# Optimization experiments

Measured on AMD Instinct MI355X. Metric: run time of the kernel, lower is better.

The kernel has to match this reference:

```python
import jax, jax.numpy as jnp
import numpy as np

BS, SEQ, D, H = 2, 2048, 1024, 16
HD = D // H  # head_dim = 64


def setup_inputs() -> dict:
    key = jax.random.key(0)
    kx, kw = jax.random.split(key)
    x = jax.random.normal(kx, (BS, SEQ, D), dtype=jnp.float32)
    # qkv Linear: weight [3D, D] (xavier_normal), bias zeros
    std = float(np.sqrt(2.0 / (D + 3 * D)))
    W_qkv = jax.random.normal(kw, (3 * D, D), dtype=jnp.float32) * std
    b_qkv = jnp.zeros((3 * D,), dtype=jnp.float32)
    return {"x": x, "W_qkv": W_qkv, "b_qkv": b_qkv}


def reference(x, W_qkv, b_qkv):
    bs, seq_len, embed_dim = x.shape
    # fused QKV projection: [bs, seq, 3D]
    qkv = x @ W_qkv.T + b_qkv
    qkv = qkv.reshape(bs, seq_len, 3, H, HD)
    qkv = jnp.transpose(qkv, (2, 0, 3, 1, 4))  # [3, bs, H, seq, HD]
    Q, K, V = qkv[0], qkv[1], qkv[2]
    # past_kv is None -> total_len == seq_len, past_len == 0
    scores = jnp.einsum("bhqd,bhkd->bhqk", Q, K) / jnp.sqrt(jnp.float32(HD))
    # causal mask: True above diagonal -> -inf
    mask = jnp.triu(jnp.ones((seq_len, seq_len), dtype=bool), k=1)
    scores = jnp.where(mask[None, None, :, :], -jnp.inf, scores)
    probs = jax.nn.softmax(scores, axis=-1)
    # attn_dropout = 0.0 (eval) -> identity
    out = jnp.einsum("bhqk,bhkd->bhqd", probs, V)
    out = jnp.transpose(out, (0, 2, 1, 3)).reshape(bs, seq_len, embed_dim)
    return (out, (K, V))
```

## Files before the change

kernel.cpp:

```cpp
#include <hip/hip_runtime.h>

typedef __bf16 bf16_t;
typedef __bf16 bf16x8 __attribute__((ext_vector_type(8)));
typedef float f32x4 __attribute__((ext_vector_type(4)));
typedef unsigned long long u64;

__device__ __forceinline__ unsigned short bfbits(float f) {
  unsigned u = __float_as_uint(f);
  u += 0x7fffu + ((u >> 16) & 1u);
  return (unsigned short)(u >> 16);
}
__device__ __forceinline__ bf16_t f2bf(float f) {
  unsigned short s = bfbits(f);
  union { unsigned short s; bf16_t b; } cv; cv.s = s; return cv.b;
}

__device__ __forceinline__ void gl16(const void* g, void* l) {
  __builtin_amdgcn_global_load_lds(
      (const __attribute__((address_space(1))) void*)g,
      (__attribute__((address_space(3))) void*)l,
      16, 0, 0);
}

__global__ __launch_bounds__(256) void cvt_kernel(const float* __restrict__ x,
                                                  const float* __restrict__ Wf,
                                                  bf16_t* __restrict__ xb,
                                                  bf16_t* __restrict__ wb) {
  const int i = blockIdx.x * 256 + threadIdx.x;
  const float* src; bf16_t* dst; int j;
  if (i < 524288) { j = i; src = x; dst = xb; }
  else            { j = i - 524288; src = Wf; dst = wb; }
  const float4* s = (const float4*)src + (size_t)j * 2;
  float4 a = s[0], b = s[1];
  bf16x8 o;
  o[0] = f2bf(a.x); o[1] = f2bf(a.y); o[2] = f2bf(a.z); o[3] = f2bf(a.w);
  o[4] = f2bf(b.x); o[5] = f2bf(b.y); o[6] = f2bf(b.z); o[7] = f2bf(b.w);
  const int row = j >> 7, jr = j & 127;
  const int dstc = (row << 7) + (jr & ~3) + ((jr & 3) ^ ((row >> 1) & 3));
  *((bf16x8*)dst + dstc) = o;
}

#define GEMM_K 1024
__global__ __launch_bounds__(256) void qkv_gemm(
    const bf16_t* __restrict__ A,
    const bf16_t* __restrict__ B,
    const float* __restrict__ bias,
    float* __restrict__ Ko, float* __restrict__ Vo,
    bf16_t* __restrict__ Qb, bf16_t* __restrict__ Kb,
    bf16_t* __restrict__ Vt,
    int* __restrict__ qcnt)
{
  if (blockIdx.x == 0 && threadIdx.x == 0) *qcnt = 0;
  __shared__ bf16_t lsA[3][4096];
  __shared__ bf16_t lsB[3][4096];
  const int tid = threadIdx.x;
  const int lane = tid & 63;
  const int ln = lane & 15, qd = lane >> 4;
  const int wid = tid >> 6;
  const int wm = wid & 1, wn = wid >> 1;
  const int xcd = blockIdx.x & 7;
  const int j = blockIdx.x >> 3;
  const int bn = xcd * 3 + (j % 3);
  const int bm = j / 3;
  const int m0 = bm * 128, n0 = bn * 128;
  const int qs = qd ^ ((ln >> 1) & 3);

  f32x4 acc[4][4] = {};

  const int c0 = tid, c1 = tid + 256;
  const bf16_t* ga0 = A + (size_t)(m0 + (c0 >> 2)) * GEMM_K + (c0 & 3) * 8;
  const bf16_t* ga1 = A + (size_t)(m0 + (c1 >> 2)) * GEMM_K + (c1 & 3) * 8;
  const bf16_t* gb0 = B + (size_t)(n0 + (c0 >> 2)) * GEMM_K + (c0 & 3) * 8;
  const bf16_t* gb1 = B + (size_t)(n0 + (c1 >> 2)) * GEMM_K + (c1 & 3) * 8;

#define STAGE(t, slot)                                   \
  do {                                                   \
    const int ko_ = (t) * 32;                            \
    gl16(ga0 + ko_, &lsA[(slot)][c0 * 8]);               \
    gl16(ga1 + ko_, &lsA[(slot)][c1 * 8]);               \
    gl16(gb0 + ko_, &lsB[(slot)][c0 * 8]);               \
    gl16(gb1 + ko_, &lsB[(slot)][c1 * 8]);               \
  } while (0)

#define COMPUTE(slot)                                                          \
  do {                                                                         \
    bf16x8 af[4], bf[4];                                                       \
    _Pragma("unroll")                                                          \
    for (int mi = 0; mi < 4; ++mi)                                             \
      af[mi] = *(const bf16x8*)&lsA[(slot)][(wm * 64 + mi * 16 + ln) * 32 + qs * 8]; \
    _Pragma("unroll")                                                          \
    for (int ni = 0; ni < 4; ++ni)                                             \
      bf[ni] = *(const bf16x8*)&lsB[(slot)][(wn * 64 + ni * 16 + ln) * 32 + qs * 8]; \
    _Pragma("unroll")                                                          \
    for (int mi = 0; mi < 4; ++mi)                                             \
      _Pragma("unroll")                                                        \
      for (int ni = 0; ni < 4; ++ni)                                           \
        acc[mi][ni] = __builtin_amdgcn_mfma_f32_16x16x32_bf16(af[mi], bf[ni], acc[mi][ni], 0, 0, 0); \
  } while (0)

#define WAITBAR(n)                                        \
  do {                                                    \
    asm volatile("s_waitcnt vmcnt(" #n ")" ::: "memory"); \
    __builtin_amdgcn_s_barrier();                         \
  } while (0)

  STAGE(0, 0);
  STAGE(1, 1);
#pragma unroll
  for (int t = 0; t < 30; ++t) {
    WAITBAR(4);
    STAGE(t + 2, (t + 2) % 3);
    COMPUTE(t % 3);
  }
  WAITBAR(4); COMPUTE(0);
  WAITBAR(0); COMPUTE(1);

#undef STAGE
#undef COMPUTE
#undef WAITBAR

  const int sec = n0 >> 10;
#pragma unroll
  for (int mi = 0; mi < 4; ++mi) {
#pragma unroll
    for (int ni = 0; ni < 4; ++ni) {
      const int colg = n0 + wn * 64 + ni * 16 + ln;
      const float bv = bias[colg];
      const int cc = colg & 1023, h = cc >> 6, hd = cc & 63;
      if (sec == 2) {
        unsigned u[4];
#pragma unroll
        for (int r = 0; r < 4; ++r) {
          const int mg = m0 + wm * 64 + mi * 16 + qd * 4 + r;
          const int b = mg >> 11, s = mg & 2047;
          const float val = acc[mi][ni][r] + bv;
          Vo[((size_t)((b * 16 + h) * 2048 + s)) * 64 + hd] = val;
          u[r] = __float_as_uint(val);
        }
        const int mg0 = m0 + wm * 64 + mi * 16 + qd * 4;
        const int b0 = mg0 >> 11, s0 = mg0 & 2047;
        const unsigned lo = (u[1] & 0xFFFF0000u) | (u[0] >> 16);
        const unsigned hi = (u[3] & 0xFFFF0000u) | (u[2] >> 16);
        const size_t vb = (size_t)(b0 * 16 + h) * 131072 + (size_t)(s0 >> 6) * 4096 +
                          (size_t)hd * 64 + ((((s0 >> 3) & 7) ^ (hd & 7)) << 3) + (s0 & 7);
        *(u64*)&Vt[vb] = ((u64)hi << 32) | lo;
      } else {
#pragma unroll
        for (int r = 0; r < 4; ++r) {
          const int mg = m0 + wm * 64 + mi * 16 + qd * 4 + r;
          const int b = mg >> 11, s = mg & 2047;
          const float val = acc[mi][ni][r] + bv;
          const int bhi = b * 16 + h;
          const size_t sidx = (size_t)bhi * 131072 + (size_t)(s >> 6) * 4096 +
                              (size_t)(s & 63) * 64 + (((hd >> 3) ^ (s & 7)) << 3) + (hd & 7);
          if (sec == 0) {
            Qb[sidx] = f2bf(val * 0.18033688f);
          } else {
            Ko[((size_t)(bhi * 2048 + s)) * 64 + hd] = val;
            Kb[sidx] = f2bf(val);
          }
        }
      }
    }
  }
}

__global__ __launch_bounds__(256) void attn_kernel(
    const bf16_t* __restrict__ Qb,
    const bf16_t* __restrict__ Kb,
    const bf16_t* __restrict__ Vt,
    float* __restrict__ Out,
    int* __restrict__ qcnt)
{
  __shared__ bf16_t lq[4096];
  __shared__ bf16_t lk[8192];
  __shared__ bf16_t lv[8192];
  __shared__ bf16_t lp[4096];
  __shared__ int task_sh;
  const int tid = threadIdx.x;
  const int lane = tid & 63, ln = lane & 15, qd = lane >> 4;
  const int w = tid >> 6;
  const int l7 = ln & 7;

  for (;;) {
    __syncthreads();
    if (tid == 0) task_sh = atomicAdd(qcnt, 1);
    __syncthreads();
    const int task = task_sh;
    if (task >= 1024) break;
    const int qi = 31 - (task >> 5);
    const int bh = task & 31;
    const int b = bh >> 4, h = bh & 15;

    const bf16_t* qbase = Qb + (size_t)bh * 131072 + (size_t)qi * 4096;
    const bf16_t* kbase = Kb + (size_t)bh * 131072;
    const bf16_t* vbase = Vt + (size_t)bh * 131072;

#pragma unroll
    for (int i = 0; i < 2; ++i) {
      const int cc = tid + i * 256;
      gl16(qbase + cc * 8, &lq[cc * 8]);
    }
#pragma unroll
    for (int i = 0; i < 4; ++i) {
      const int cc = tid + i * 256;
      gl16(kbase + cc * 8, &lk[cc * 8]);
      gl16(vbase + cc * 8, &lv[cc * 8]);
    }
    __syncthreads();

    bf16x8 afq[2];
    {
      const int row = w * 16 + ln;
#pragma unroll
      for (int kk = 0; kk < 2; ++kk)
        afq[kk] = *(const bf16x8*)&lq[row * 64 + (((kk * 4 + qd) ^ l7) << 3)];
    }

    f32x4 oc[4] = {};
    float lsum = 0.f;
    const int qg = qi * 64 + w * 16 + ln;
    const int q = w * 16 + ln;

    for (int kt = 0; kt <= qi; ++kt) {
      const int st = kt >> 1, h2 = kt & 1;
      if (h2 == 0 && st > 0) {
        __syncthreads();
#pragma unroll
        for (int i = 0; i < 4; ++i) {
          const int cc = tid + i * 256;
          gl16(kbase + (size_t)st * 8192 + cc * 8, &lk[cc * 8]);
          gl16(vbase + (size_t)st * 8192 + cc * 8, &lv[cc * 8]);
        }
        __syncthreads();
      }
      const bool diag = (kt == qi);
      const int lofs = h2 * 4096;

      f32x4 sa[4] = {};
#pragma unroll
      for (int kk = 0; kk < 2; ++kk) {
        bf16x8 ak[4];
#pragma unroll
        for (int ki = 0; ki < 4; ++ki)
          ak[ki] = *(const bf16x8*)&lk[lofs + (ki * 16 + ln) * 64 + (((kk * 4 + qd) ^ l7) << 3)];
#pragma unroll
        for (int ki = 0; ki < 4; ++ki)
          sa[ki] = __builtin_amdgcn_mfma_f32_16x16x32_bf16(ak[ki], afq[kk], sa[ki], 0, 0, 0);
      }

#pragma unroll
      for (int ki = 0; ki < 4; ++ki) {
        const int kb0 = kt * 64 + ki * 16 + qd * 4;
        float p0 = __builtin_amdgcn_exp2f(sa[ki][0]);
        float p1 = __builtin_amdgcn_exp2f(sa[ki][1]);
        float p2 = __builtin_amdgcn_exp2f(sa[ki][2]);
        float p3 = __builtin_amdgcn_exp2f(sa[ki][3]);
        if (diag) {
          if (kb0 + 0 > qg) p0 = 0.f;
          if (kb0 + 1 > qg) p1 = 0.f;
          if (kb0 + 2 > qg) p2 = 0.f;
          if (kb0 + 3 > qg) p3 = 0.f;
        }
        lsum += (p0 + p1) + (p2 + p3);
        const unsigned lo = (__float_as_uint(p1) & 0xFFFF0000u) | (__float_as_uint(p0) >> 16);
        const unsigned hi = (__float_as_uint(p3) & 0xFFFF0000u) | (__float_as_uint(p2) >> 16);
        const int g = (ki * 2 + (qd >> 1)) ^ l7;
        *(u64*)&lp[q * 64 + g * 8 + (qd & 1) * 4] = ((u64)hi << 32) | lo;
      }

#pragma unroll
      for (int kk = 0; kk < 2; ++kk) {
        bf16x8 afp, bfv[4];
        afp = *(const bf16x8*)&lp[q * 64 + (((kk * 4 + qd) ^ l7) << 3)];
#pragma unroll
        for (int ni = 0; ni < 4; ++ni)
          bfv[ni] = *(const bf16x8*)&lv[lofs + (ni * 16 + ln) * 64 + (((kk * 4 + qd) ^ l7) << 3)];
#pragma unroll
        for (int ni = 0; ni < 4; ++ni)
          oc[ni] = __builtin_amdgcn_mfma_f32_16x16x32_bf16(afp, bfv[ni], oc[ni], 0, 0, 0);
      }
    }

    float ls = lsum;
    ls += __shfl_xor(ls, 16);
    ls += __shfl_xor(ls, 32);
#pragma unroll
    for (int r = 0; r < 4; ++r) {
      const float lval = __shfl(ls, qd * 4 + r);
      const float inv = 1.0f / lval;
      const int rowq = qi * 64 + w * 16 + qd * 4 + r;
#pragma unroll
      for (int ni = 0; ni < 4; ++ni) {
        const int colh = ni * 16 + ln;
        Out[(size_t)(b * 2048 + rowq) * 1024 + h * 64 + colh] = oc[ni][r] * inv;
      }
    }
  }
}

extern "C" void kernel_launch(void* const* d_in, const int* in_sizes, int n_in,
                              void* d_out, int out_size, void* d_ws, size_t ws_size,
                              hipStream_t stream) {
  const float* x = (const float*)d_in[0];
  const float* W = (const float*)d_in[1];
  const float* bq = (const float*)d_in[2];
  float* out = (float*)d_out;
  float* Ko = out + 4194304;
  float* Vo = out + 8388608;
  char* ws = (char*)d_ws;
  bf16_t* xb = (bf16_t*)ws;
  bf16_t* wb = (bf16_t*)(ws + 8388608);
  bf16_t* Qb = (bf16_t*)(ws + 14680064);
  bf16_t* Kb = (bf16_t*)(ws + 23068672);
  bf16_t* Vt = (bf16_t*)(ws + 31457280);
  int*    qcnt = (int*)(ws + 39845888);

  hipLaunchKernelGGL(cvt_kernel, dim3(3584), dim3(256), 0, stream, x, W, xb, wb);
  hipLaunchKernelGGL(qkv_gemm, dim3(768), dim3(256), 0, stream, xb, wb, bq, Ko, Vo, Qb, Kb, Vt, qcnt);
  hipLaunchKernelGGL(attn_kernel, dim3(768), dim3(256), 0, stream, Qb, Kb, Vt, out, qcnt);
}
```

Baseline: 169.5 us.

## Prefetch next K/V stage into registers while computing current stage

The attention loop now iterates over 128-key stages. It issues global loads for the next stage's K and V tiles into registers before computing on the current LDS tile, then writes those registers to LDS between barriers. This overlaps global memory latency with MFMA and exp work, replacing the previous blocking global-to-LDS load and sync at each stage boundary. The cost is 32 extra VGPRs for the prefetch buffers, which may reduce occupancy, plus explicit register-to-LDS stores in place of direct global_load_lds.

```diff
diff --git a/kernel.cpp b/kernel.cpp
--- a/kernel.cpp
+++ b/kernel.cpp
@@ -221,64 +221,84 @@
     float lsum = 0.f;
     const int qg = qi * 64 + w * 16 + ln;
     const int q = w * 16 + ln;
-
-    for (int kt = 0; kt <= qi; ++kt) {
-      const int st = kt >> 1, h2 = kt & 1;
-      if (h2 == 0 && st > 0) {
-        __syncthreads();
+    const int nst = (qi >> 1) + 1;
+
+    for (int st = 0; st < nst; ++st) {
+      float4 kr[4], vr[4];
+      if (st + 1 < nst) {
+        const size_t off = (size_t)(st + 1) * 8192;
 #pragma unroll
         for (int i = 0; i < 4; ++i) {
           const int cc = tid + i * 256;
-          gl16(kbase + (size_t)st * 8192 + cc * 8, &lk[cc * 8]);
-          gl16(vbase + (size_t)st * 8192 + cc * 8, &lv[cc * 8]);
-        }
-        __syncthreads();
-      }
-      const bool diag = (kt == qi);
-      const int lofs = h2 * 4096;
-
-      f32x4 sa[4] = {};
-#pragma unroll
-      for (int kk = 0; kk < 2; ++kk) {
-        bf16x8 ak[4];
-#pragma unroll
-        for (int ki = 0; ki < 4; ++ki)
-          ak[ki] = *(const bf16x8*)&lk[lofs + (ki * 16 + ln) * 64 + (((kk * 4 + qd) ^ l7) << 3)];
-#pragma unroll
-        for (int ki = 0; ki < 4; ++ki)
-          sa[ki] = __builtin_amdgcn_mfma_f32_16x16x32_bf16(ak[ki], afq[kk], sa[ki], 0, 0, 0);
-      }
-
-#pragma unroll
-      for (int ki = 0; ki < 4; ++ki) {
-        const int kb0 = kt * 64 + ki * 16 + qd * 4;
-        float p0 = __builtin_amdgcn_exp2f(sa[ki][0]);
-        float p1 = __builtin_amdgcn_exp2f(sa[ki][1]);
-        float p2 = __builtin_amdgcn_exp2f(sa[ki][2]);
-        float p3 = __builtin_amdgcn_exp2f(sa[ki][3]);
-        if (diag) {
-          if (kb0 + 0 > qg) p0 = 0.f;
-          if (kb0 + 1 > qg) p1 = 0.f;
-          if (kb0 + 2 > qg) p2 = 0.f;
-          if (kb0 + 3 > qg) p3 = 0.f;
-        }
-        lsum += (p0 + p1) + (p2 + p3);
-        const unsigned lo = (__float_as_uint(p1) & 0xFFFF0000u) | (__float_as_uint(p0) >> 16);
-        const unsigned hi = (__float_as_uint(p3) & 0xFFFF0000u) | (__float_as_uint(p2) >> 16);
-        const int g = (ki * 2 + (qd >> 1)) ^ l7;
-        *(u64*)&lp[q * 64 + g * 8 + (qd & 1) * 4] = ((u64)hi << 32) | lo;
-      }
-
-#pragma unroll
-      for (int kk = 0; kk < 2; ++kk) {
-        bf16x8 afp, bfv[4];
-        afp = *(const bf16x8*)&lp[q * 64 + (((kk * 4 + qd) ^ l7) << 3)];
-#pragma unroll
-        for (int ni = 0; ni < 4; ++ni)
-          bfv[ni] = *(const bf16x8*)&lv[lofs + (ni * 16 + ln) * 64 + (((kk * 4 + qd) ^ l7) << 3)];
-#pragma unroll
-        for (int ni = 0; ni < 4; ++ni)
-          oc[ni] = __builtin_amdgcn_mfma_f32_16x16x32_bf16(afp, bfv[ni], oc[ni], 0, 0, 0);
+          kr[i] = *(const float4*)(kbase + off + cc * 8);
+          vr[i] = *(const float4*)(vbase + off + cc * 8);
+        }
+        asm volatile("" ::: "memory");
+      }
+
+#pragma unroll
+      for (int h2 = 0; h2 < 2; ++h2) {
+        const int kt = st * 2 + h2;
+        if (kt > qi) break;
+        const bool diag = (kt == qi);
+        const int lofs = h2 * 4096;
+
+        f32x4 sa[4] = {};
+#pragma unroll
+        for (int kk = 0; kk < 2; ++kk) {
+          bf16x8 ak[4];
+#pragma unroll
+          for (int ki = 0; ki < 4; ++ki)
+            ak[ki] = *(const bf16x8*)&lk[lofs + (ki * 16 + ln) * 64 + (((kk * 4 + qd) ^ l7) << 3)];
+#pragma unroll
+          for (int ki = 0; ki < 4; ++ki)
+            sa[ki] = __builtin_amdgcn_mfma_f32_16x16x32_bf16(ak[ki], afq[kk], sa[ki], 0, 0, 0);
+        }
+
+#pragma unroll
+        for (int ki = 0; ki < 4; ++ki) {
+          const int kb0 = kt * 64 + ki * 16 + qd * 4;
+          float p0 = __builtin_amdgcn_exp2f(sa[ki][0]);
+          float p1 = __builtin_amdgcn_exp2f(sa[ki][1]);
+          float p2 = __builtin_amdgcn_exp2f(sa[ki][2]);
+          float p3 = __builtin_amdgcn_exp2f(sa[ki][3]);
+          if (diag) {
+            if (kb0 + 0 > qg) p0 = 0.f;
+            if (kb0 + 1 > qg) p1 = 0.f;
+            if (kb0 + 2 > qg) p2 = 0.f;
+            if (kb0 + 3 > qg) p3 = 0.f;
+          }
+          lsum += (p0 + p1) + (p2 + p3);
+          const unsigned lo = (__float_as_uint(p1) & 0xFFFF0000u) | (__float_as_uint(p0) >> 16);
+          const unsigned hi = (__float_as_uint(p3) & 0xFFFF0000u) | (__float_as_uint(p2) >> 16);
+          const int g = (ki * 2 + (qd >> 1)) ^ l7;
+          *(u64*)&lp[q * 64 + g * 8 + (qd & 1) * 4] = ((u64)hi << 32) | lo;
+        }
+
+#pragma unroll
+        for (int kk = 0; kk < 2; ++kk) {
+          bf16x8 afp, bfv[4];
+          afp = *(const bf16x8*)&lp[q * 64 + (((kk * 4 + qd) ^ l7) << 3)];
+#pragma unroll
+          for (int ni = 0; ni < 4; ++ni)
+            bfv[ni] = *(const bf16x8*)&lv[lofs + (ni * 16 + ln) * 64 + (((kk * 4 + qd) ^ l7) << 3)];
+#pragma unroll
+          for (int ni = 0; ni < 4; ++ni)
+            oc[ni] = __builtin_amdgcn_mfma_f32_16x16x32_bf16(afp, bfv[ni], oc[ni], 0, 0, 0);
+        }
+      }
+
+      if (st + 1 < nst) {
+        __builtin_amdgcn_s_barrier();
+        asm volatile("s_waitcnt vmcnt(0)" ::: "memory");
+#pragma unroll
+        for (int i = 0; i < 4; ++i) {
+          const int cc = tid + i * 256;
+          *(float4*)&lk[cc * 8] = kr[i];
+          *(float4*)&lv[cc * 8] = vr[i];
+        }
+        asm volatile("s_waitcnt lgkmcnt(0)" ::: "memory");
+        __builtin_amdgcn_s_barrier();
       }
     }
 
```

Result: slower. 230.8 us (+36.1%).
